# Performance work log

Measured on AMD Instinct MI355X. Metric: run time of the kernel, lower is better.

## Reference

```python
import jax, jax.numpy as jnp
from jax import lax
import numpy as np

K = 2            # kernel size
C_RES = 128      # residual channels (== input channels)
C_DIL = 256      # dilation channels
C_SKIP = 256     # skip channels
DIL = 4          # dilation rate


def causal_conv1d(x, w, b, dilation):
    # x: [B, T, Cin], w: [K, Cin, Cout] (WIO), causal left-pad
    pad = (w.shape[0] - 1) * dilation
    y = lax.conv_general_dilated(
        x, w, window_strides=(1,), padding=[(pad, 0)],
        rhs_dilation=(dilation,), dimension_numbers=("NWC", "WIO", "NWC"))
    return y + b


def setup_inputs() -> dict:
    key = jax.random.key(0)
    ks = jax.random.split(key, 9)
    B, T = 8, 16384
    def glorot(k, shape):
        fan_in = shape[0] * shape[1]
        fan_out = shape[0] * shape[2]
        lim = np.sqrt(6.0 / (fan_in + fan_out)).astype(np.float32)
        return jax.random.uniform(k, shape, jnp.float32, -lim, lim)
    return {
        "inputs": jax.random.normal(ks[0], (B, T, C_RES), jnp.float32),
        "w_tanh": glorot(ks[1], (K, C_RES, C_DIL)),
        "b_tanh": jnp.zeros((C_DIL,), jnp.float32),
        "w_sig": glorot(ks[2], (K, C_RES, C_DIL)),
        "b_sig": jnp.zeros((C_DIL,), jnp.float32),
        "w_res": glorot(ks[3], (1, C_DIL, C_RES)),
        "b_res": jnp.zeros((C_RES,), jnp.float32),
        "w_skip": glorot(ks[4], (1, C_DIL, C_SKIP)),
        "b_skip": jnp.zeros((C_SKIP,), jnp.float32),
    }


def reference(inputs, w_tanh, b_tanh, w_sig, b_sig, w_res, b_res, w_skip, b_skip):
    tanh_out = jnp.tanh(causal_conv1d(inputs, w_tanh, b_tanh, DIL))
    sig_out = jax.nn.sigmoid(causal_conv1d(inputs, w_sig, b_sig, DIL))
    merged = tanh_out * sig_out                      # [B, T, C_DIL]
    # 1x1 convs as matmuls
    res_out = jnp.einsum("btc,cd->btd", merged, w_res[0]) + b_res + inputs
    skip_out = jnp.einsum("btc,cd->btd", merged, w_skip[0]) + b_skip
    return res_out, skip_out
```

## Files before the change

### kernel.cpp

```cpp
#include <hip/hip_runtime.h>

#define T_LEN 16384
#define N_TOT 131072
#define ROWS 64
#define XROWS 68
#define XPITCH 136
#define MPITCH 264

typedef __attribute__((ext_vector_type(8))) short short8;
typedef __attribute__((ext_vector_type(4))) short short4v;
typedef __attribute__((ext_vector_type(4))) float floatx4;
typedef unsigned short ushort_t;

__device__ __forceinline__ ushort_t f2bf(float f) {
    unsigned int u = __float_as_uint(f);
    u += 0x7fffu + ((u >> 16) & 1u);
    return (ushort_t)(u >> 16);
}

__global__ void repack_w(const float* __restrict__ w_tanh,
                         const float* __restrict__ w_sig,
                         const float* __restrict__ w_res,
                         const float* __restrict__ w_skip,
                         ushort_t* __restrict__ w1,
                         ushort_t* __restrict__ w2) {
    int i = blockIdx.x * 256 + threadIdx.x;
    if (i < 8 * 512 * 32) {
        int kk = i & 31;
        int n  = (i >> 5) & 511;
        int kc = i >> 14;
        int k  = kc * 32 + kk;
        int tap = (k < 128) ? 1 : 0;
        int cin = k & 127;
        float v = (n < 256) ? w_tanh[(tap * 128 + cin) * 256 + n]
                            : w_sig [(tap * 128 + cin) * 256 + (n - 256)];
        w1[i] = f2bf(v);
    } else {
        int j = i - 8 * 512 * 32;
        if (j < 8 * 384 * 32) {
            int kk = j & 31;
            int n  = (j >> 5) % 384;
            int kc = j / (384 * 32);
            int k  = kc * 32 + kk;
            float v = (n < 128) ? w_res[k * 128 + n]
                                : w_skip[k * 256 + (n - 128)];
            w2[j] = f2bf(v);
        }
    }
}

__global__ __launch_bounds__(512)
void fused_block(const float* __restrict__ x,
                 const float* __restrict__ b_tanh,
                 const float* __restrict__ b_sig,
                 const float* __restrict__ b_res,
                 const float* __restrict__ b_skip,
                 const ushort_t* __restrict__ w1,
                 const ushort_t* __restrict__ w2,
                 float* __restrict__ out) {
    __shared__ ushort_t xbuf[XROWS * XPITCH];
    __shared__ ushort_t mbuf[ROWS * MPITCH];

    const int tid = threadIdx.x;
    const int n0  = blockIdx.x * ROWS;
    const int t0  = n0 & (T_LEN - 1);

    for (int idx = tid; idx < XROWS * 32; idx += 512) {
        int r  = idx >> 5;
        int c4 = (idx & 31) << 2;
        int t  = t0 - 4 + r;
        short4v s;
        if (t >= 0) {
            floatx4 v = *(const floatx4*)(x + (size_t)(n0 - 4 + r) * 128 + c4);
            s = short4v{(short)f2bf(v[0]), (short)f2bf(v[1]),
                        (short)f2bf(v[2]), (short)f2bf(v[3])};
        } else {
            s = short4v{0, 0, 0, 0};
        }
        *(short4v*)(xbuf + r * XPITCH + c4) = s;
    }
    __syncthreads();

    const int w    = tid >> 6;
    const int lane = tid & 63;
    const int quad = lane >> 4;
    const int l16  = lane & 15;

    const floatx4 zero4 = {0.f, 0.f, 0.f, 0.f};

    floatx4 acc_t[4][2], acc_s[4][2];
    #pragma unroll
    for (int rt = 0; rt < 4; ++rt)
        #pragma unroll
        for (int ct = 0; ct < 2; ++ct) { acc_t[rt][ct] = zero4; acc_s[rt][ct] = zero4; }

    #pragma unroll
    for (int kc = 0; kc < 8; ++kc) {
        const int colb = (kc & 3) * 32 + quad * 8;
        const int roff = (kc < 4) ? 4 : 0;
        short8 a[4];
        #pragma unroll
        for (int rt = 0; rt < 4; ++rt)
            a[rt] = *(const short8*)(xbuf + (rt * 16 + l16 + roff) * XPITCH + colb);
        short8 bt[2], bs[2];
        #pragma unroll
        for (int ct = 0; ct < 2; ++ct) {
            int n_t = 32 * w + ct * 16 + l16;
            bt[ct] = *(const short8*)(w1 + ((kc * 512 + n_t)       * 32) + quad * 8);
            bs[ct] = *(const short8*)(w1 + ((kc * 512 + n_t + 256) * 32) + quad * 8);
        }
        #pragma unroll
        for (int rt = 0; rt < 4; ++rt)
            #pragma unroll
            for (int ct = 0; ct < 2; ++ct) {
                acc_t[rt][ct] = __builtin_amdgcn_mfma_f32_16x16x32_bf16(a[rt], bt[ct], acc_t[rt][ct], 0, 0, 0);
                acc_s[rt][ct] = __builtin_amdgcn_mfma_f32_16x16x32_bf16(a[rt], bs[ct], acc_s[rt][ct], 0, 0, 0);
            }
    }

    #pragma unroll
    for (int ct = 0; ct < 2; ++ct) {
        int c = 32 * w + ct * 16 + l16;
        float btb = b_tanh[c];
        float bsb = b_sig[c];
        #pragma unroll
        for (int rt = 0; rt < 4; ++rt)
            #pragma unroll
            for (int i = 0; i < 4; ++i) {
                float pt = acc_t[rt][ct][i] + btb;
                float ps = acc_s[rt][ct][i] + bsb;
                float e2 = __expf(2.0f * pt);
                float th = 1.0f - 2.0f / (e2 + 1.0f);
                float sg = 1.0f / (1.0f + __expf(-ps));
                int row = rt * 16 + quad * 4 + i;
                mbuf[row * MPITCH + c] = f2bf(th * sg);
            }
    }
    __syncthreads();

    floatx4 acc2[4][3];
    #pragma unroll
    for (int rt = 0; rt < 4; ++rt)
        #pragma unroll
        for (int ct = 0; ct < 3; ++ct) acc2[rt][ct] = zero4;

    #pragma unroll
    for (int kc = 0; kc < 8; ++kc) {
        short8 a[4];
        #pragma unroll
        for (int rt = 0; rt < 4; ++rt)
            a[rt] = *(const short8*)(mbuf + (rt * 16 + l16) * MPITCH + kc * 32 + quad * 8);
        short8 b[3];
        #pragma unroll
        for (int ct = 0; ct < 3; ++ct) {
            int n2 = 48 * w + ct * 16 + l16;
            b[ct] = *(const short8*)(w2 + (kc * 384 + n2) * 32 + quad * 8);
        }
        #pragma unroll
        for (int rt = 0; rt < 4; ++rt)
            #pragma unroll
            for (int ct = 0; ct < 3; ++ct)
                acc2[rt][ct] = __builtin_amdgcn_mfma_f32_16x16x32_bf16(a[rt], b[ct], acc2[rt][ct], 0, 0, 0);
    }

    #pragma unroll
    for (int ct = 0; ct < 3; ++ct) {
        int col = 48 * w + ct * 16 + l16;
        if (col < 128) {
            float bb = b_res[col];
            #pragma unroll
            for (int rt = 0; rt < 4; ++rt)
                #pragma unroll
                for (int i = 0; i < 4; ++i) {
                    int row = rt * 16 + quad * 4 + i;
                    size_t g = (size_t)(n0 + row);
                    out[g * 128 + col] = acc2[rt][ct][i] + bb + x[g * 128 + col];
                }
        } else {
            int c2 = col - 128;
            float bb = b_skip[c2];
            #pragma unroll
            for (int rt = 0; rt < 4; ++rt)
                #pragma unroll
                for (int i = 0; i < 4; ++i) {
                    int row = rt * 16 + quad * 4 + i;
                    size_t g = (size_t)(n0 + row);
                    out[(size_t)N_TOT * 128 + g * 256 + c2] = acc2[rt][ct][i] + bb;
                }
        }
    }
}

extern "C" void kernel_launch(void* const* d_in, const int* in_sizes, int n_in,
                              void* d_out, int out_size, void* d_ws, size_t ws_size,
                              hipStream_t stream) {
    const float* x      = (const float*)d_in[0];
    const float* w_tanh = (const float*)d_in[1];
    const float* b_tanh = (const float*)d_in[2];
    const float* w_sig  = (const float*)d_in[3];
    const float* b_sig  = (const float*)d_in[4];
    const float* w_res  = (const float*)d_in[5];
    const float* b_res  = (const float*)d_in[6];
    const float* w_skip = (const float*)d_in[7];
    const float* b_skip = (const float*)d_in[8];

    ushort_t* w1 = (ushort_t*)d_ws;
    ushort_t* w2 = w1 + 8 * 512 * 32;
    float* out = (float*)d_out;

    repack_w<<<896, 256, 0, stream>>>(w_tanh, w_sig, w_res, w_skip, w1, w2);
    fused_block<<<N_TOT / ROWS, 512, 0, stream>>>(x, b_tanh, b_sig, b_res, b_skip, w1, w2, out);
}
```

Baseline: 392.6 us.

## Cut register and LDS pressure to raise occupancy in fused WaveNet block

Splits the tanh and sigmoid gate GEMMs into two sequential passes and stores the tanh pre-activations as packed bf16 while the sigmoid pass runs, halving live accumulators. xbuf and mbuf are aliased into one shared buffer, with an extra barrier before mbuf is written. The second GEMM is processed in two row halves, and launch bounds request 6 blocks per CU. The goal is higher occupancy to hide memory latency. The cost is that the x tile is read from LDS twice, and rounding tanh pre-activations to bf16 adds some extra error.

```diff
diff --git a/kernel.cpp b/kernel.cpp
--- a/kernel.cpp
+++ b/kernel.cpp
@@ -12,6 +12,9 @@
 typedef __attribute__((ext_vector_type(4))) float floatx4;
 typedef unsigned short ushort_t;
 
+__device__ __forceinline__ float bf2f(ushort_t u) {
+    return __uint_as_float(((unsigned int)u) << 16);
+}
 __device__ __forceinline__ ushort_t f2bf(float f) {
     unsigned int u = __float_as_uint(f);
     u += 0x7fffu + ((u >> 16) & 1u);
@@ -49,7 +52,7 @@
     }
 }
 
-__global__ __launch_bounds__(512)
+__global__ __launch_bounds__(512, 6)
 void fused_block(const float* __restrict__ x,
                  const float* __restrict__ b_tanh,
                  const float* __restrict__ b_sig,
@@ -58,8 +61,9 @@
                  const ushort_t* __restrict__ w1,
                  const ushort_t* __restrict__ w2,
                  float* __restrict__ out) {
-    __shared__ ushort_t xbuf[XROWS * XPITCH];
-    __shared__ ushort_t mbuf[ROWS * MPITCH];
+    __shared__ ushort_t smem[ROWS * MPITCH];
+    ushort_t* xbuf = smem;
+    ushort_t* mbuf = smem;
 
     const int tid = threadIdx.x;
     const int n0  = blockIdx.x * ROWS;
@@ -88,11 +92,9 @@
 
     const floatx4 zero4 = {0.f, 0.f, 0.f, 0.f};
 
-    floatx4 acc_t[4][2], acc_s[4][2];
-    #pragma unroll
-    for (int rt = 0; rt < 4; ++rt)
-        #pragma unroll
-        for (int ct = 0; ct < 2; ++ct) { acc_t[rt][ct] = zero4; acc_s[rt][ct] = zero4; }
+    floatx4 acc[4][2];
+    #pragma unroll
+    for (int rt = 0; rt < 4; ++rt) { acc[rt][0] = zero4; acc[rt][1] = zero4; }
 
     #pragma unroll
     for (int kc = 0; kc < 8; ++kc) {
@@ -102,21 +104,49 @@
         #pragma unroll
         for (int rt = 0; rt < 4; ++rt)
             a[rt] = *(const short8*)(xbuf + (rt * 16 + l16 + roff) * XPITCH + colb);
-        short8 bt[2], bs[2];
+        short8 bt[2];
+        #pragma unroll
+        for (int ct = 0; ct < 2; ++ct)
+            bt[ct] = *(const short8*)(w1 + ((kc * 512 + 32 * w + ct * 16 + l16) * 32) + quad * 8);
+        #pragma unroll
+        for (int rt = 0; rt < 4; ++rt)
+            #pragma unroll
+            for (int ct = 0; ct < 2; ++ct)
+                acc[rt][ct] = __builtin_amdgcn_mfma_f32_16x16x32_bf16(a[rt], bt[ct], acc[rt][ct], 0, 0, 0);
+    }
+
+    unsigned int pk_t[4][2][2];
+    #pragma unroll
+    for (int rt = 0; rt < 4; ++rt)
         #pragma unroll
         for (int ct = 0; ct < 2; ++ct) {
-            int n_t = 32 * w + ct * 16 + l16;
-            bt[ct] = *(const short8*)(w1 + ((kc * 512 + n_t)       * 32) + quad * 8);
-            bs[ct] = *(const short8*)(w1 + ((kc * 512 + n_t + 256) * 32) + quad * 8);
-        }
-        #pragma unroll
-        for (int rt = 0; rt < 4; ++rt)
-            #pragma unroll
-            for (int ct = 0; ct < 2; ++ct) {
-                acc_t[rt][ct] = __builtin_amdgcn_mfma_f32_16x16x32_bf16(a[rt], bt[ct], acc_t[rt][ct], 0, 0, 0);
-                acc_s[rt][ct] = __builtin_amdgcn_mfma_f32_16x16x32_bf16(a[rt], bs[ct], acc_s[rt][ct], 0, 0, 0);
-            }
-    }
+            pk_t[rt][ct][0] = (unsigned int)f2bf(acc[rt][ct][0]) | ((unsigned int)f2bf(acc[rt][ct][1]) << 16);
+            pk_t[rt][ct][1] = (unsigned int)f2bf(acc[rt][ct][2]) | ((unsigned int)f2bf(acc[rt][ct][3]) << 16);
+        }
+
+    #pragma unroll
+    for (int rt = 0; rt < 4; ++rt) { acc[rt][0] = zero4; acc[rt][1] = zero4; }
+
+    #pragma unroll
+    for (int kc = 0; kc < 8; ++kc) {
+        const int colb = (kc & 3) * 32 + quad * 8;
+        const int roff = (kc < 4) ? 4 : 0;
+        short8 a[4];
+        #pragma unroll
+        for (int rt = 0; rt < 4; ++rt)
+            a[rt] = *(const short8*)(xbuf + (rt * 16 + l16 + roff) * XPITCH + colb);
+        short8 bs[2];
+        #pragma unroll
+        for (int ct = 0; ct < 2; ++ct)
+            bs[ct] = *(const short8*)(w1 + ((kc * 512 + 256 + 32 * w + ct * 16 + l16) * 32) + quad * 8);
+        #pragma unroll
+        for (int rt = 0; rt < 4; ++rt)
+            #pragma unroll
+            for (int ct = 0; ct < 2; ++ct)
+                acc[rt][ct] = __builtin_amdgcn_mfma_f32_16x16x32_bf16(a[rt], bs[ct], acc[rt][ct], 0, 0, 0);
+    }
+
+    __syncthreads();
 
     #pragma unroll
     for (int ct = 0; ct < 2; ++ct) {
@@ -127,8 +157,8 @@
         for (int rt = 0; rt < 4; ++rt)
             #pragma unroll
             for (int i = 0; i < 4; ++i) {
-                float pt = acc_t[rt][ct][i] + btb;
-                float ps = acc_s[rt][ct][i] + bsb;
+                float pt = bf2f((ushort_t)(pk_t[rt][ct][i >> 1] >> ((i & 1) * 16))) + btb;
+                float ps = acc[rt][ct][i] + bsb;
                 float e2 = __expf(2.0f * pt);
                 float th = 1.0f - 2.0f / (e2 + 1.0f);
                 float sg = 1.0f / (1.0f + __expf(-ps));
@@ -138,55 +168,56 @@
     }
     __syncthreads();
 
-    floatx4 acc2[4][3];
-    #pragma unroll
-    for (int rt = 0; rt < 4; ++rt)
-        #pragma unroll
-        for (int ct = 0; ct < 3; ++ct) acc2[rt][ct] = zero4;
-
-    #pragma unroll
-    for (int kc = 0; kc < 8; ++kc) {
-        short8 a[4];
-        #pragma unroll
-        for (int rt = 0; rt < 4; ++rt)
-            a[rt] = *(const short8*)(mbuf + (rt * 16 + l16) * MPITCH + kc * 32 + quad * 8);
-        short8 b[3];
+    #pragma unroll
+    for (int half = 0; half < 2; ++half) {
+        floatx4 acc2[2][3];
+        #pragma unroll
+        for (int rt = 0; rt < 2; ++rt)
+            #pragma unroll
+            for (int ct = 0; ct < 3; ++ct) acc2[rt][ct] = zero4;
+
+        #pragma unroll
+        for (int kc = 0; kc < 8; ++kc) {
+            short8 a[2];
+            #pragma unroll
+            for (int rt = 0; rt < 2; ++rt)
+                a[rt] = *(const short8*)(mbuf + ((half * 2 + rt) * 16 + l16) * MPITCH + kc * 32 + quad * 8);
+            short8 b[3];
+            #pragma unroll
+            for (int ct = 0; ct < 3; ++ct)
+                b[ct] = *(const short8*)(w2 + (kc * 384 + 48 * w + ct * 16 + l16) * 32 + quad * 8);
+            #pragma unroll
+            for (int rt = 0; rt < 2; ++rt)
+                #pragma unroll
+                for (int ct = 0; ct < 3; ++ct)
+                    acc2[rt][ct] = __builtin_amdgcn_mfma_f32_16x16x32_bf16(a[rt], b[ct], acc2[rt][ct], 0, 0, 0);
+        }
+
         #pragma unroll
         for (int ct = 0; ct < 3; ++ct) {
-            int n2 = 48 * w + ct * 16 + l16;
-            b[ct] = *(const short8*)(w2 + (kc * 384 + n2) * 32 + quad * 8);
-        }
-        #pragma unroll
-        for (int rt = 0; rt < 4; ++rt)
-            #pragma unroll
-            for (int ct = 0; ct < 3; ++ct)
-                acc2[rt][ct] = __builtin_amdgcn_mfma_f32_16x16x32_bf16(a[rt], b[ct], acc2[rt][ct], 0, 0, 0);
-    }
-
-    #pragma unroll
-    for (int ct = 0; ct < 3; ++ct) {
-        int col = 48 * w + ct * 16 + l16;
-        if (col < 128) {
-            float bb = b_res[col];
-            #pragma unroll
-            for (int rt = 0; rt < 4; ++rt)
+            int col = 48 * w + ct * 16 + l16;
+            if (col < 128) {
+                float bb = b_res[col];
                 #pragma unroll
-                for (int i = 0; i < 4; ++i) {
-                    int row = rt * 16 + quad * 4 + i;
-                    size_t g = (size_t)(n0 + row);
-                    out[g * 128 + col] = acc2[rt][ct][i] + bb + x[g * 128 + col];
-                }
-        } else {
-            int c2 = col - 128;
-            float bb = b_skip[c2];
-            #pragma unroll
-            for (int rt = 0; rt < 4; ++rt)
+                for (int rt = 0; rt < 2; ++rt)
+                    #pragma unroll
+                    for (int i = 0; i < 4; ++i) {
+                        int row = (half * 2 + rt) * 16 + quad * 4 + i;
+                        size_t g = (size_t)(n0 + row);
+                        out[g * 128 + col] = acc2[rt][ct][i] + bb + x[g * 128 + col];
+                    }
+            } else {
+                int c2 = col - 128;
+                float bb = b_skip[c2];
                 #pragma unroll
-                for (int i = 0; i < 4; ++i) {
-                    int row = rt * 16 + quad * 4 + i;
-                    size_t g = (size_t)(n0 + row);
-                    out[(size_t)N_TOT * 128 + g * 256 + c2] = acc2[rt][ct][i] + bb;
-                }
+                for (int rt = 0; rt < 2; ++rt)
+                    #pragma unroll
+                    for (int i = 0; i < 4; ++i) {
+                        int row = (half * 2 + rt) * 16 + quad * 4 + i;
+                        size_t g = (size_t)(n0 + row);
+                        out[(size_t)N_TOT * 128 + g * 256 + c2] = acc2[rt][ct][i] + bb;
+                    }
+            }
         }
     }
 }
```

After: 613.1 us. +56.2%, slower.
